# Performance work log

Hardware: AMD Instinct MI355X
Metric: run time of the kernel (lower is better)

Reference implementation:

```python
import jax, jax.numpy as jnp
import numpy as np
from jax import lax

BLOCK = 64      # block_size
OVERLAP = 16
NITER = 64      # Niter init kwarg; loop runs min(1000, Niter)
L = 0.24        # diffusion step size
K = 0.03        # exp(logk), logk = log(0.03)
DEPS = 0.1
FFT_STEPS = 10
THRESH = 0.1    # uniform-region variance threshold


def _g(x):
    # g(x) = 1 / (1 + |x^2| / K^2)
    return 1.0 / (1.0 + jnp.abs(x * x) / (K * K))


def _avgpool3(x):
    # F.avg_pool2d(x, 3, stride=1, padding=1) with count_include_pad=True (divide by 9)
    s = lax.reduce_window(x, 0.0, lax.add, (1, 1, 3, 3), (1, 1, 1, 1),
                          [(0, 0), (0, 0), (1, 1), (1, 1)])
    return s / 9.0


def _fft_diffuse_block(block, bcv, bch):
    cv_mean = bcv.mean()
    ch_mean = bch.mean()
    h, w = block.shape[2], block.shape[3]
    ky = jnp.arange(h, dtype=block.dtype)[:, None] * (2.0 * np.pi / h)      # [h,1]
    kx = jnp.arange(w // 2 + 1, dtype=block.dtype)[None, :] * (2.0 * np.pi / w)  # [1,w//2+1]
    op = (1.0 - 2.0 * L * (cv_mean * (1.0 - jnp.cos(ky)) + ch_mean * (1.0 - jnp.cos(kx)))) ** FFT_STEPS
    return jnp.fft.irfft2(jnp.fft.rfft2(block) * op, s=(h, w))


def _forward(guide, initial):
    # depth shift for stability (torch code branches on initial.min() <= deps)
    shift = jnp.where(initial.min() <= DEPS, DEPS, 0.0).astype(initial.dtype)
    depth = initial + shift

    # diffusion coefficients from guide: cv [B,1,H-1,W], ch [B,1,H,W-1]
    cv = _g(jnp.mean(jnp.abs(guide[:, :, 1:, :] - guide[:, :, :-1, :]), axis=1, keepdims=True))
    ch = _g(jnp.mean(jnp.abs(guide[:, :, :, 1:] - guide[:, :, :, :-1]), axis=1, keepdims=True))

    # identify_uniform_regions (local variance via avg pools); original torch code
    # broadcasts shapes (H-1,W) & (H,W-1) which errors -- we crop to common (H-1,W-1)
    cv_var = _avgpool3(cv ** 2) - _avgpool3(cv) ** 2
    ch_var = _avgpool3(ch ** 2) - _avgpool3(ch) ** 2
    uniform = ((cv_var[:, :, :, :-1] < THRESH) & (ch_var[:, :, :-1, :] < THRESH)).astype(depth.dtype)

    B, C, H, W = depth.shape
    step = BLOCK - OVERLAP
    # sequential per-block FFT diffusion with overlap blending (blocks read
    # depth updated by previous blocks, so order matters)
    for b in range(B):
        for y in range(0, H, step):
            for x in range(0, W, step):
                y_end = min(y + BLOCK, H)
                x_end = min(x + BLOCK, W)
                bh, bw = y_end - y, x_end - x
                block = depth[b:b + 1, :, y:y_end, x:x_end]
                bcv = cv[b:b + 1, :, y:y_end - 1, x:x_end]
                bch = ch[b:b + 1, :, y:y_end, x:x_end - 1]
                bun = uniform[b:b + 1, :, y:y_end, x:x_end]  # clips at edges (H-1,W-1)
                cond = bun.mean() > 0.7
                newb = _fft_diffuse_block(block, bcv, bch)
                if y > 0 or x > 0:
                    blend_y = jnp.ones((bh,), depth.dtype)
                    if y > 0:
                        r = jnp.arange(bh)
                        blend_y = jnp.where(r < min(OVERLAP, bh), r.astype(depth.dtype) / OVERLAP, blend_y)
                    blend_x = jnp.ones((bw,), depth.dtype)
                    if x > 0:
                        r = jnp.arange(bw)
                        blend_x = jnp.where(r < min(OVERLAP, bw), r.astype(depth.dtype) / OVERLAP, blend_x)
                    blend = (blend_y[:, None] * blend_x[None, :])[None, None]
                    cand = block * (1.0 - blend) + newb * blend
                else:
                    cand = newb
                region = jnp.where(cond, cand, block)
                depth = depth.at[b:b + 1, :, y:y_end, x:x_end].set(region)

    # explicit anisotropic diffusion stencil, serial data dependence -> lax.scan
    def diffuse_step(I, _):
        dv = I[:, :, 1:, :] - I[:, :, :-1, :]
        dh = I[:, :, :, 1:] - I[:, :, :, :-1]  # computed before vertical update (as in torch)
        tv = L * cv * dv
        I = I.at[:, :, 1:, :].add(-tv).at[:, :, :-1, :].add(tv)
        th = L * ch * dh
        I = I.at[:, :, :, 1:].add(-th).at[:, :, :, :-1].add(th)
        return I, None

    depth, _ = lax.scan(diffuse_step, depth, None, length=min(1000, NITER))
    y_pred = depth - shift
    return y_pred, cv, ch


def setup_inputs() -> dict:
    key = jax.random.key(0)
    k1, k2 = jax.random.split(key)
    guide = jax.random.uniform(k1, (2, 3, 512, 512), dtype=jnp.float32)
    initial = jax.random.uniform(k2, (2, 1, 512, 512), dtype=jnp.float32)
    return {"guide": guide, "initial": initial}


def reference(guide, initial):
    # returns (y_pred, cv, ch) matching {'y_pred':..., 'cv':..., 'ch':...}
    return _forward(guide, initial)
```

## Files before the change

kernel.cpp:

```cpp
#include <hip/hip_runtime.h>
#include <stdint.h>

#define LDIFF 0.24f

constexpr int H = 512, W = 512, NB = 2;
constexpr int HW = H * W;
constexpr int N_D = NB * HW;
constexpr int CVH = 511, CVW = 512;
constexpr int CHH = 512, CHW = 511;
constexpr int N_CV = NB * CVH * CVW;
constexpr int NBLKS = 11;
constexpr int NBT = NB * 121;

__device__ inline float ldc(const float* p) {
    return __hip_atomic_load(p, __ATOMIC_RELAXED, __HIP_MEMORY_SCOPE_AGENT);
}
__device__ inline void stc(float* p, float v) {
    __hip_atomic_store(p, v, __ATOMIC_RELAXED, __HIP_MEMORY_SCOPE_AGENT);
}
__device__ inline int ldci(const int* p) {
    return __hip_atomic_load(p, __ATOMIC_RELAXED, __HIP_MEMORY_SCOPE_AGENT);
}
__device__ inline void stci(int* p, int v) {
    __hip_atomic_store(p, v, __ATOMIC_RELAXED, __HIP_MEMORY_SCOPE_AGENT);
}
template <int SLP>
__device__ inline void poll_ge(const int* p, int v) {
    while (ldci(p) < v) __builtin_amdgcn_s_sleep(SLP);
}

__device__ inline float rot_a(float x) {
    return __int_as_float(__builtin_amdgcn_update_dpp(0, __float_as_int(x), 0x134, 0xf, 0xf, false));
}
__device__ inline float rot_b(float x) {
    return __int_as_float(__builtin_amdgcn_update_dpp(0, __float_as_int(x), 0x13c, 0xf, 0xf, false));
}
__device__ inline float sh_a(float x) {
    return __int_as_float(__builtin_amdgcn_update_dpp(0, __float_as_int(x), 0x130, 0xf, 0xf, true));
}
__device__ inline float sh_b(float x) {
    return __int_as_float(__builtin_amdgcn_update_dpp(0, __float_as_int(x), 0x138, 0xf, 0xf, true));
}

__global__ __launch_bounds__(256) void kall(
    const float* __restrict__ guide, const float* __restrict__ initial,
    float* __restrict__ cv, float* __restrict__ ch,
    float* __restrict__ D, float* __restrict__ T0, float* __restrict__ T1,
    float* __restrict__ ypred, int* __restrict__ sync_)
{
    __shared__ float cvT[73 * 74];
    __shared__ float chT[73 * 74];
    __shared__ float xT[2][4][64];
    __shared__ float xB[2][4][64];
    __shared__ float red[12];
    __shared__ float prmS[3];

    int* wflag = sync_;
    int* dflag = sync_ + 4096;

    const int blk = blockIdx.x;
    const int i = blk / NBLKS, j = blk % NBLKS;
    const int b = blockIdx.y;
    const int tid = threadIdx.x;
    const int lane = tid & 63, wv = tid >> 6;
    const int r0 = wv * 16;
    const int me = b * 121 + blk;

    const int y0 = i * 48, x0 = j * 48;
    const int y1 = min(y0 + 64, 512), x1 = min(x0 + 64, 512);
    const int bh = y1 - y0, bw = x1 - x0;
    const int yb = y0 - 8, xb = x0 - 8;
    const float kinv = 1.0f / (0.03f * 0.03f);

    const float* gb = guide + (size_t)b * 3 * HW;
    for (int p = tid; p < 73 * 73; p += 256) {
        int rr = p / 73, cc2 = p - rr * 73;
        int y = yb + rr, x = xb + cc2;
        float cvv = 0.0f, chv = 0.0f;
        if (y >= 0 && y < 512 && x >= 0 && x < 512) {
            const float* g = gb + y * W + x;
            float g0 = g[0], g1 = g[HW], g2 = g[2 * HW];
            if (y < 511) {
                float d = (fabsf(g[W] - g0) + fabsf(g[HW + W] - g1) + fabsf(g[2 * HW + W] - g2)) * (1.0f / 3.0f);
                cvv = 1.0f / (1.0f + d * d * kinv);
            }
            if (x < 511) {
                float d = (fabsf(g[1] - g0) + fabsf(g[HW + 1] - g1) + fabsf(g[2 * HW + 1] - g2)) * (1.0f / 3.0f);
                chv = 1.0f / (1.0f + d * d * kinv);
            }
        }
        cvT[rr * 74 + cc2] = cvv;
        chT[rr * 74 + cc2] = chv;
    }
    __syncthreads();

    {
        int rcv = min(y0 + 48, CVH) - y0, ccv = min(x0 + 48, CVW) - x0;
        float* cvo = cv + b * CVH * CVW;
        for (int p = tid; p < rcv * ccv; p += 256) {
            int r = p / ccv, c = p - r * ccv;
            cvo[(y0 + r) * CVW + x0 + c] = cvT[(r + 8) * 74 + c + 8];
        }
        int rch = min(y0 + 48, CHH) - y0, cch = min(x0 + 48, CHW) - x0;
        float* cho = ch + b * CHH * CHW;
        for (int p = tid; p < rch * cch; p += 256) {
            int r = p / cch, c = p - r * cch;
            cho[(y0 + r) * CHW + x0 + c] = chT[(r + 8) * 74 + c + 8];
        }
    }

    float scv = 0.f, sch = 0.f, sun = 0.f;
    {
        int n = (bh - 1) * bw;
        for (int p = tid; p < n; p += 256) { int r = p / bw, c = p - r * bw; scv += cvT[(r + 8) * 74 + c + 8]; }
    }
    {
        int cols = bw - 1, n = bh * cols;
        for (int p = tid; p < n; p += 256) { int r = p / cols, c = p - r * cols; sch += chT[(r + 8) * 74 + c + 8]; }
    }
    const int ur = min(y1, 511) - y0, uc = min(x1, 511) - x0;
    {
        int n = ur * uc;
        for (int p = tid; p < n; p += 256) {
            int r = p / uc, c = p - r * uc;
            float s1 = 0.f, s2 = 0.f, t1 = 0.f, t2 = 0.f;
            #pragma unroll
            for (int dy = 0; dy < 3; dy++)
                #pragma unroll
                for (int dx = 0; dx < 3; dx++) {
                    float v = cvT[(r + 7 + dy) * 74 + c + 7 + dx]; s1 += v; s2 += v * v;
                    float w2 = chT[(r + 7 + dy) * 74 + c + 7 + dx]; t1 += w2; t2 += w2 * w2;
                }
            float m = s1 * (1.0f / 9.0f);
            float vcv = s2 * (1.0f / 9.0f) - m * m;
            m = t1 * (1.0f / 9.0f);
            float vch = t2 * (1.0f / 9.0f) - m * m;
            if (vcv < 0.1f && vch < 0.1f) sun += 1.f;
        }
    }
    #pragma unroll
    for (int m = 1; m < 64; m <<= 1) {
        scv += __shfl_xor(scv, m);
        sch += __shfl_xor(sch, m);
        sun += __shfl_xor(sun, m);
    }
    if (lane == 0) { red[wv * 3] = scv; red[wv * 3 + 1] = sch; red[wv * 3 + 2] = sun; }
    __syncthreads();
    if (tid == 0) {
        float a0 = red[0] + red[3] + red[6] + red[9];
        float a1 = red[1] + red[4] + red[7] + red[10];
        float a2 = red[2] + red[5] + red[8] + red[11];
        prmS[0] = a0 / (float)((bh - 1) * bw);
        prmS[1] = a1 / (float)(bh * (bw - 1));
        prmS[2] = (a2 / (float)(ur * uc) > 0.7f) ? 1.0f : 0.0f;
    }
    __syncthreads();

    int prb = __builtin_amdgcn_update_dpp(0, lane, 0x134, 0xf, 0xf, false);
    const bool dirL = (prb == ((lane + 63) & 63));

    const bool cond = prmS[2] > 0.5f;
    const float a = LDIFF * prmS[0], bc = LDIFF * prmS[1];
    float* Db = D + b * HW;
    const float* ini = initial + b * HW;

    const int mh = bh - 1, mw = bw - 1;
    const int ccw = lane & mw;

    if (!cond) {
        #pragma unroll
        for (int k = 0; k < 16; k++) {
            int r = r0 + k;
            if (r < bh && (i == 0 || r >= 16) && lane < bw && (j == 0 || lane >= 16)) {
                int ad = (y0 + r) * W + x0 + lane;
                stc(&Db[ad], ini[ad]);
            }
        }
        asm volatile("s_waitcnt vmcnt(0)" ::: "memory");
        __syncthreads();
        if (tid == 0) stci(&wflag[me * 16], 1);
    } else {
        float u[16], orig[16];
        int addr[16]; bool fD[16];
        #pragma unroll
        for (int k = 0; k < 16; k++) {
            int rr = (r0 + k) & mh;
            addr[k] = (y0 + rr) * W + x0 + ccw;
            fD[k] = (i > 0 && rr < 16) || (j > 0 && ccw < 16);
            if (!fD[k]) orig[k] = ini[addr[k]];
        }
        if (tid < 3) {
            int di = (tid == 0) ? i : i - 1;
            int dj = (tid == 0) ? j - 1 : ((tid == 1) ? j : j + 1);
            if (di >= 0 && dj >= 0 && dj < NBLKS)
                poll_ge<1>(&wflag[(b * 121 + di * NBLKS + dj) * 16], 1);
        }
        __syncthreads();
        #pragma unroll
        for (int k = 0; k < 16; k++) if (fD[k]) orig[k] = ldc(&Db[addr[k]]);
        #pragma unroll
        for (int k = 0; k < 16; k++) u[k] = orig[k];

        int bs = 0;
        for (int it = 0; it < 10; it++) {
            xT[bs][wv][lane] = u[0];
            xB[bs][wv][lane] = u[15];
            __syncthreads();
            float ub = xB[bs][(wv + 3) & 3][lane];
            float ut = xT[bs][(wv + 1) & 3][lane];
            float nu[16];
            #pragma unroll
            for (int k = 0; k < 16; k++) {
                float up = (k == 0) ? ub : u[k - 1];
                float dn = (k == 15) ? ut : u[k + 1];
                float hsum = rot_a(u[k]) + rot_b(u[k]);
                nu[k] = u[k] + a * (up + dn - 2.0f * u[k]) + bc * (hsum - 2.0f * u[k]);
            }
            #pragma unroll
            for (int k = 0; k < 16; k++) u[k] = nu[k];
            bs ^= 1;
        }

        #pragma unroll
        for (int k = 0; k < 16; k++) {
            int r = r0 + k;
            if (r < bh && lane < bw) {
                int rr = r;
                float byw = (y0 > 0 && rr < 16) ? (float)rr * (1.0f / 16.0f) : 1.0f;
                float bxw = (x0 > 0 && lane < 16) ? (float)lane * (1.0f / 16.0f) : 1.0f;
                float wgt = byw * bxw;
                stc(&Db[(y0 + r) * W + x0 + lane], orig[k] * (1.0f - wgt) + u[k] * wgt);
            }
        }
        asm volatile("s_waitcnt vmcnt(0)" ::: "memory");
        __syncthreads();
        if (tid == 0) stci(&wflag[me * 16], 1);
    }

    const int cx = xb + lane;
    const int gxc = min(max(cx, 0), 511);
    float cvr[16], chr[16], chl[16];
    int gyA[16];
    #pragma unroll
    for (int k = 0; k < 16; k++) {
        int cy = yb + r0 + k;
        gyA[k] = min(max(cy, 0), 511);
        cvr[k] = cvT[(r0 + k) * 74 + lane];
        chr[k] = chT[(r0 + k) * 74 + lane];
        chl[k] = dirL ? sh_a(chr[k]) : sh_b(chr[k]);
    }
    const float cvm1 = (wv == 0) ? 0.0f : cvT[(r0 - 1) * 74 + lane];

    float* Tb0 = T0 + b * HW;
    float* Tb1 = T1 + b * HW;
    float* ypb = ypred + b * HW;
    const bool cok = (lane >= 8 && lane < 56 && xb + lane < 512);

    for (int t = 1; t <= 8; t++) {
        if (tid < 9) {
            int di = tid / 3 - 1, dj = tid % 3 - 1;
            int ni = i + di, nj = j + dj;
            if (ni >= 0 && ni < NBLKS && nj >= 0 && nj < NBLKS && (di | dj) != 0) {
                int nb = (b * 121 + ni * NBLKS + nj) * 16;
                if (t == 1) poll_ge<2>(&wflag[nb], 1);
                else        poll_ge<2>(&dflag[nb], t - 1);
            }
        }
        if (t == 1 && tid == 9) poll_ge<2>(&wflag[me * 16], 1);
        __syncthreads();
        const float* src = (t == 1) ? Db : (((t - 1) & 1) ? Tb1 : Tb0);
        float u[16];
        #pragma unroll
        for (int k = 0; k < 16; k++) u[k] = ldc(&src[gyA[k] * W + gxc]);

        int bs = 0;
        for (int it = 0; it < 8; it++) {
            xT[bs][wv][lane] = u[0];
            xB[bs][wv][lane] = u[15];
            __syncthreads();
            float ub = (wv > 0) ? xB[bs][wv - 1][lane] : u[0];
            float ut = (wv < 3) ? xT[bs][wv + 1][lane] : u[15];
            float V[16];
            #pragma unroll
            for (int k = 0; k < 16; k++) {
                float up = (k == 0) ? ub : u[k - 1];
                float dn = (k == 15) ? ut : u[k + 1];
                float cup = (k == 0) ? cvm1 : cvr[k - 1];
                V[k] = u[k] + LDIFF * cvr[k] * (dn - u[k]) - LDIFF * cup * (u[k] - up);
            }
            #pragma unroll
            for (int k = 0; k < 16; k++) {
                float rA = rot_a(V[k]);
                float rB = rot_b(V[k]);
                float lf = dirL ? rA : rB;
                float rt = dirL ? rB : rA;
                u[k] = V[k] + LDIFF * chr[k] * (rt - V[k]) - LDIFF * chl[k] * (V[k] - lf);
            }
            bs ^= 1;
        }

        if (t < 8) {
            float* dst = (t & 1) ? Tb1 : Tb0;
            if (cok) {
                #pragma unroll
                for (int k = 0; k < 16; k++) {
                    int r = r0 + k;
                    if (r >= 8 && r < 56) {
                        int y = yb + r;
                        if (y < 512) stc(&dst[y * W + xb + lane], u[k]);
                    }
                }
            }
            asm volatile("s_waitcnt vmcnt(0)" ::: "memory");
            __syncthreads();
            if (tid == 0) stci(&dflag[me * 16], t);
        } else {
            if (cok) {
                #pragma unroll
                for (int k = 0; k < 16; k++) {
                    int r = r0 + k;
                    if (r >= 8 && r < 56) {
                        int y = yb + r;
                        if (y < 512) ypb[y * W + xb + lane] = u[k];
                    }
                }
            }
        }
    }
}

extern "C" void kernel_launch(void* const* d_in, const int* in_sizes, int n_in,
                              void* d_out, int out_size, void* d_ws, size_t ws_size,
                              hipStream_t stream) {
    const float* guide   = (const float*)d_in[0];
    const float* initial = (const float*)d_in[1];
    float* y_pred = (float*)d_out;
    float* cv = y_pred + N_D;
    float* ch = cv + N_CV;

    uint8_t* w = (uint8_t*)d_ws;
    int* sync_ = (int*)w;
    float* D  = (float*)(w + 32768);
    float* T0 = (float*)(w + 32768 + (size_t)N_D * 4);
    float* T1 = (float*)(w + 32768 + (size_t)2 * N_D * 4);

    (void)hipMemsetAsync(sync_, 0, 32768, stream);
    kall<<<dim3(121, NB), 256, 0, stream>>>(guide, initial, cv, ch, D, T0, T1, y_pred, sync_);
}
```

Before: 322.1 us.

## Use per-wavefront completion flags and ballot-based parallel polling for block dependencies

Each wavefront now publishes its own completion flag after its stores, so the block-wide barrier before signalling is gone. Consumers poll the needed neighbour flags in parallel across the lanes of one wavefront using a ballot, replacing serial polling by individual threads. The FFT-stage dependency only waits on the specific wavefronts that wrote the overlapping rows or columns, which can start dependent blocks earlier. The flag area grows to 128 KB and must be cleared every launch, and the sleep intervals change.

```diff
diff --git a/kernel.cpp b/kernel.cpp
--- a/kernel.cpp
+++ b/kernel.cpp
@@ -23,10 +23,6 @@
 }
 __device__ inline void stci(int* p, int v) {
     __hip_atomic_store(p, v, __ATOMIC_RELAXED, __HIP_MEMORY_SCOPE_AGENT);
-}
-template <int SLP>
-__device__ inline void poll_ge(const int* p, int v) {
-    while (ldci(p) < v) __builtin_amdgcn_s_sleep(SLP);
 }
 
 __device__ inline float rot_a(float x) {
@@ -56,7 +52,7 @@
     __shared__ float prmS[3];
 
     int* wflag = sync_;
-    int* dflag = sync_ + 4096;
+    int* dflag = sync_ + 16384;
 
     const int blk = blockIdx.x;
     const int i = blk / NBLKS, j = blk % NBLKS;
@@ -177,8 +173,7 @@
             }
         }
         asm volatile("s_waitcnt vmcnt(0)" ::: "memory");
-        __syncthreads();
-        if (tid == 0) stci(&wflag[me * 16], 1);
+        if (lane == 0) stci(&wflag[me * 64 + wv * 16], 1);
     } else {
         float u[16], orig[16];
         int addr[16]; bool fD[16];
@@ -189,11 +184,23 @@
             fD[k] = (i > 0 && rr < 16) || (j > 0 && ccw < 16);
             if (!fD[k]) orig[k] = ini[addr[k]];
         }
-        if (tid < 3) {
-            int di = (tid == 0) ? i : i - 1;
-            int dj = (tid == 0) ? j - 1 : ((tid == 1) ? j : j + 1);
-            if (di >= 0 && dj >= 0 && dj < NBLKS)
-                poll_ge<1>(&wflag[(b * 121 + di * NBLKS + dj) * 16], 1);
+        if (wv == 0) {
+            bool need = false;
+            const int* fp = &wflag[me * 64];
+            if (lane < 3) {
+                if (j > 0) { need = true; fp = &wflag[(b * 121 + i * NBLKS + j - 1) * 64 + (lane + 1) * 16]; }
+            } else if (lane == 3) {
+                if (i > 0) { need = true; fp = &wflag[(b * 121 + (i - 1) * NBLKS + j) * 64 + 3 * 16]; }
+            } else if (lane == 4) {
+                if (i > 0 && j < 10) { need = true; fp = &wflag[(b * 121 + (i - 1) * NBLKS + j + 1) * 64 + 3 * 16]; }
+            } else if (lane == 5) {
+                if (i > 0 && j > 0) { need = true; fp = &wflag[(b * 121 + (i - 1) * NBLKS + j - 1) * 64 + 3 * 16]; }
+            }
+            while (true) {
+                int v = need ? ldci(fp) : 1;
+                if (__ballot(v == 0) == 0) break;
+                __builtin_amdgcn_s_sleep(0);
+            }
         }
         __syncthreads();
         #pragma unroll
@@ -225,17 +232,16 @@
         for (int k = 0; k < 16; k++) {
             int r = r0 + k;
             if (r < bh && lane < bw) {
-                int rr = r;
-                float byw = (y0 > 0 && rr < 16) ? (float)rr * (1.0f / 16.0f) : 1.0f;
+                float byw = (y0 > 0 && r < 16) ? (float)r * (1.0f / 16.0f) : 1.0f;
                 float bxw = (x0 > 0 && lane < 16) ? (float)lane * (1.0f / 16.0f) : 1.0f;
                 float wgt = byw * bxw;
                 stc(&Db[(y0 + r) * W + x0 + lane], orig[k] * (1.0f - wgt) + u[k] * wgt);
             }
         }
         asm volatile("s_waitcnt vmcnt(0)" ::: "memory");
-        __syncthreads();
-        if (tid == 0) stci(&wflag[me * 16], 1);
-    }
+        if (lane == 0) stci(&wflag[me * 64 + wv * 16], 1);
+    }
+    __syncthreads();
 
     const int cx = xb + lane;
     const int gxc = min(max(cx, 0), 511);
@@ -257,16 +263,37 @@
     const bool cok = (lane >= 8 && lane < 56 && xb + lane < 512);
 
     for (int t = 1; t <= 8; t++) {
-        if (tid < 9) {
-            int di = tid / 3 - 1, dj = tid % 3 - 1;
-            int ni = i + di, nj = j + dj;
-            if (ni >= 0 && ni < NBLKS && nj >= 0 && nj < NBLKS && (di | dj) != 0) {
-                int nb = (b * 121 + ni * NBLKS + nj) * 16;
-                if (t == 1) poll_ge<2>(&wflag[nb], 1);
-                else        poll_ge<2>(&dflag[nb], t - 1);
-            }
-        }
-        if (t == 1 && tid == 9) poll_ge<2>(&wflag[me * 16], 1);
+        if (wv == 0) {
+            bool need = false;
+            const int* fp = &wflag[me * 64];
+            int thr = 1;
+            if (t == 1) {
+                if (lane < 36) {
+                    int nb = lane >> 2;
+                    int di = nb / 3 - 1, dj = nb % 3 - 1;
+                    int ni = i + di, nj = j + dj;
+                    if ((di | dj) != 0 && ni >= 0 && ni < NBLKS && nj >= 0 && nj < NBLKS) {
+                        need = true;
+                        fp = &wflag[(b * 121 + ni * NBLKS + nj) * 64 + (lane & 3) * 16];
+                    }
+                }
+            } else {
+                thr = t - 1;
+                if (lane < 9) {
+                    int di = lane / 3 - 1, dj = lane % 3 - 1;
+                    int ni = i + di, nj = j + dj;
+                    if ((di | dj) != 0 && ni >= 0 && ni < NBLKS && nj >= 0 && nj < NBLKS) {
+                        need = true;
+                        fp = &dflag[(b * 121 + ni * NBLKS + nj) * 16];
+                    }
+                }
+            }
+            while (true) {
+                int v = need ? ldci(fp) : 0x7fffffff;
+                if (__ballot(v < thr) == 0) break;
+                __builtin_amdgcn_s_sleep(8);
+            }
+        }
         __syncthreads();
         const float* src = (t == 1) ? Db : (((t - 1) & 1) ? Tb1 : Tb0);
         float u[16];
@@ -340,10 +367,10 @@
 
     uint8_t* w = (uint8_t*)d_ws;
     int* sync_ = (int*)w;
-    float* D  = (float*)(w + 32768);
-    float* T0 = (float*)(w + 32768 + (size_t)N_D * 4);
-    float* T1 = (float*)(w + 32768 + (size_t)2 * N_D * 4);
-
-    (void)hipMemsetAsync(sync_, 0, 32768, stream);
+    float* D  = (float*)(w + 131072);
+    float* T0 = (float*)(w + 131072 + (size_t)N_D * 4);
+    float* T1 = (float*)(w + 131072 + (size_t)2 * N_D * 4);
+
+    (void)hipMemsetAsync(sync_, 0, 131072, stream);
     kall<<<dim3(121, NB), 256, 0, stream>>>(guide, initial, cv, ch, D, T0, T1, y_pred, sync_);
 }
```

Result: no change. 321.9 us (-0.0%).
